# Kernel tuning notes

Hardware: AMD Instinct MI355X
Metric: run time of the kernel (lower is better)

The kernel has to match this reference:

```python
import jax, jax.numpy as jnp
import numpy as np

B, T, N, F_, KH, D, KD = 16, 12, 325, 64, 4, 16, 3  # batch, time, nodes, feat, heads, head_dim, diffusion steps
H = KH // 2
EPS = 1e-5


def setup_inputs() -> dict:
    key = jax.random.key(0)
    ks = jax.random.split(key, 16)
    lin = lambda k: (jax.random.normal(k, (F_, F_), jnp.float32) * 0.02)
    return {
        "x": jax.random.normal(ks[0], (B, T, N, F_), jnp.float32),
        "A": jax.random.uniform(ks[1], (KD, N, N), jnp.float32),
        "AT": jax.random.uniform(ks[2], (KD, N, N), jnp.float32),
        "Wq": lin(ks[3]), "bq": jnp.zeros((F_,), jnp.float32),
        "Wk": lin(ks[4]), "bk": jnp.zeros((F_,), jnp.float32),
        "Wks": lin(ks[5]), "bks": jnp.zeros((F_,), jnp.float32),
        "Wv": lin(ks[6]), "bv": jnp.zeros((F_,), jnp.float32),
        "Wvs": lin(ks[7]), "bvs": jnp.zeros((F_,), jnp.float32),
        "Wdi": jax.random.normal(ks[8], (H, KD, N, N), jnp.float32) * 0.05,
        "Wdo": jax.random.normal(ks[9], (H, KD, N, N), jnp.float32) * 0.05,
        "Wf1": lin(ks[10]), "bf1": jnp.zeros((F_,), jnp.float32),
        "Wf2": lin(ks[11]), "bf2": jnp.zeros((F_,), jnp.float32),
        "g_ln": jnp.ones((F_,), jnp.float32), "b_ln": jnp.zeros((F_,), jnp.float32),
    }


def _heads(y):
    # [B,T,N,F] -> [KH,B,T,N,D]  (torch.split along -1 then stack on dim 0)
    return y.reshape(B, T, N, KH, D).transpose(3, 0, 1, 2, 4)


def _attn_half(q, k, ks_, v, vs, bias):
    # q,k,ks_,v,vs: [H,B,T,N,D]; bias: [H,1,1,N,N]
    scale = 1.0 / jnp.sqrt(jnp.float32(D))
    e = jnp.einsum('hbtnd,hbtmd->hbtnm', q, k) * scale + bias
    es = jax.nn.sigmoid((q * ks_).sum(-1, keepdims=True) * scale)  # [H,B,T,N,1]
    e = e - e.max(-1, keepdims=True)
    ex = jnp.exp(e)
    a = ex / (es + ex.sum(-1, keepdims=True))  # sigmoid-augmented softmax
    out = jnp.einsum('hbtnm,hbtmd->hbtnd', a, v)
    return out + vs - a.sum(-1, keepdims=True) * vs


def reference(x, A, AT, Wq, bq, Wk, bk, Wks, bks, Wv, bv, Wvs, bvs,
              Wdi, Wdo, Wf1, bf1, Wf2, bf2, g_ln, b_ln):
    q = _heads(x @ Wq.T + bq)
    k = _heads(x @ Wk.T + bk)
    ks_ = _heads(x @ Wks.T + bks)
    v = _heads(x @ Wv.T + bv)
    vs = _heads(x @ Wvs.T + bvs)

    # DCN graph-diffusion bias: sum_j W[h,j] * A[j] -> [H,1,1,N,N]
    bias_i = jnp.einsum('hknm,knm->hnm', Wdi, A)[:, None, None]
    bias_o = jnp.einsum('hknm,knm->hnm', Wdo, AT)[:, None, None]

    vi = _attn_half(q[:H], k[:H], ks_[:H], v[:H], vs[:H], bias_i)
    vo = _attn_half(q[H:], k[H:], ks_[H:], v[H:], vs[H:], bias_o)

    val = jnp.concatenate([vi, vo], 0)  # [KH,B,T,N,D]
    val = val.transpose(1, 2, 3, 0, 4).reshape(B, T, N, F_)

    h = jax.nn.gelu(val @ Wf1.T + bf1, approximate=False) @ Wf2.T + bf2
    h = h + x

    mu = h.mean(-1, keepdims=True)
    var = ((h - mu) ** 2).mean(-1, keepdims=True)
    return g_ln * (h - mu) / jnp.sqrt(var + EPS) + b_ln
```

## Files before the change

### kernel.cpp

```cpp
#include <hip/hip_runtime.h>
#include <hip/hip_bf16.h>
#include <math.h>

#define NN 325
#define FD 64
#define KH 4
#define DH 16
#define BT 192
#define NN2 (NN*NN)
#define PST (NN*DH)
#define VTS  352
#define VSLICE (16*VTS)
#define HSTR 72
#define PLW 352
#define NPROJ 975
#define NBIAS 1848
#define NPAD  (KH*BT)
#define LOG2E 1.44269504088896f

typedef __attribute__((ext_vector_type(8))) short short8;
typedef __attribute__((ext_vector_type(4))) float f32x4;

union U8 { uint4 u; short8 s; ushort us[8]; };
__device__ inline short8 lds8(const ushort* p){ U8 t; t.u = *(const uint4*)p; return t.s; }
__device__ inline float b2f(ushort v){ return __uint_as_float(((unsigned)v) << 16); }
__device__ inline ushort f2b(float f){
  unsigned u = __float_as_uint(f);
  u += 0x7fff + ((u >> 16) & 1);
  return (ushort)(u >> 16);
}
__device__ inline unsigned pk2(float a, float b){
  union { __hip_bfloat162 h; unsigned u; } t;
  t.h = __float22bfloat162_rn(float2{a, b});
  return t.u;
}
__device__ inline short8 cvt8(const float* p){
  float4 u = ((const float4*)p)[0], v = ((const float4*)p)[1];
  U8 t;
  t.us[0]=f2b(u.x); t.us[1]=f2b(u.y); t.us[2]=f2b(u.z); t.us[3]=f2b(u.w);
  t.us[4]=f2b(v.x); t.us[5]=f2b(v.y); t.us[6]=f2b(v.z); t.us[7]=f2b(v.w);
  return t.s;
}

__global__ __launch_bounds__(256) void wpack_kernel(
    const float* __restrict__ Wq,  const float* __restrict__ bq,
    const float* __restrict__ Wk,  const float* __restrict__ bk,
    const float* __restrict__ Wks, const float* __restrict__ bks,
    const float* __restrict__ Wv,  const float* __restrict__ bv,
    const float* __restrict__ Wvs, const float* __restrict__ bvs,
    const float* __restrict__ Wf1, const float* __restrict__ Wf2,
    ushort* __restrict__ Wcat, float* __restrict__ bcat,
    ushort* __restrict__ idT){
  int blk = blockIdx.x;
  if (blk == 7){
    for (int e = threadIdx.x; e < 672; e += 256){
      int l = e & 31, mm = l & 15, gg = l >> 4;
      U8 t;
      #pragma unroll
      for (int j = 0; j < 8; ++j) t.us[j] = (mm == gg*8 + j) ? (ushort)0x3F80 : (ushort)0;
      *(uint4*)(idT + (size_t)e*8) = t.u;
    }
    return;
  }
  const float* Ws[7] = {Wq, Wk, Wks, Wv, Wvs, Wf1, Wf2};
  const float* bs[5] = {bq, bk, bks, bv, bvs};
  int f = blk * 64 + (threadIdx.x >> 2);
  int c0 = (threadIdx.x & 3) * 8;
  const float* wr = Ws[blk] + (f & 63) * 64;
  unsigned* dst = (unsigned*)Wcat + f * 32 + c0;
  #pragma unroll
  for (int c = 0; c < 8; ++c)
    dst[c] = f2b(wr[2*(c0+c)]) | ((unsigned)f2b(wr[2*(c0+c)+1]) << 16);
  if (blk < 5 && (threadIdx.x & 3) == 0) bcat[f] = bs[blk][f & 63];
}

__global__ __launch_bounds__(256) void prep_kernel(
    const float* __restrict__ x, const ushort* __restrict__ Wcat,
    const float* __restrict__ bcat, ushort* __restrict__ proj,
    ushort* __restrict__ vt,
    const float* __restrict__ Wdi, const float* __restrict__ Wdo,
    const float* __restrict__ A,   const float* __restrict__ AT,
    ushort* __restrict__ biasB){
  int bid = blockIdx.x, tid = threadIdx.x;
  if (bid < NPROJ){
    int lane = tid & 63, wid = tid >> 6;
    int r0 = bid * 64 + wid * 16;
    int m = lane & 15, g = lane >> 4;
    int gr = r0 + m;
    int bt = gr / NN, n = gr - bt * NN;
    const float* xr = x + (size_t)gr * 64 + g * 8;
    short8 xb0 = cvt8(xr);
    short8 xb1 = cvt8(xr + 32);
    for (int ct = 0; ct < 20; ++ct){
      short8 w0 = lds8(Wcat + ((size_t)(ct*16 + m) * 64 + g * 8));
      short8 w1 = lds8(Wcat + ((size_t)(ct*16 + m) * 64 + g * 8 + 32));
      float4 b4 = *(const float4*)(bcat + ct*16 + 4*g);
      f32x4 acc = {b4.x, b4.y, b4.z, b4.w};
      acc = __builtin_amdgcn_mfma_f32_16x16x32_bf16(w0, xb0, acc, 0, 0, 0);
      acc = __builtin_amdgcn_mfma_f32_16x16x32_bf16(w1, xb1, acc, 0, 0, 0);
      if (ct >= 12 && ct < 16){
        ushort* vs = vt + (size_t)((ct-12)*BT + bt) * VSLICE + n;
        #pragma unroll
        for (int rg = 0; rg < 4; ++rg)
          vs[(size_t)(4*g + rg) * VTS] = f2b(acc[rg]);
      } else {
        float sc = (ct < 4) ? 0.25f * LOG2E : 1.0f;
        uint2 w;
        w.x = pk2(acc[0]*sc, acc[1]*sc);
        w.y = pk2(acc[2]*sc, acc[3]*sc);
        *(uint2*)(proj + ((size_t)ct * BT + bt) * PST + n*16 + 4*g) = w;
      }
    }
  } else if (bid < NPROJ + NBIAS){
    int idx = (bid - NPROJ) * 256 + tid;
    int h = idx / 118272;
    int rem = idx - h * 118272;
    int n = rem / 352, mc = rem - n * 352;
    float s = -1e30f;
    if (n < NN && mc < NN){
      int r = n * NN + mc;
      s = 0.f;
      if (h < 2){
        #pragma unroll
        for (int k = 0; k < 3; ++k) s += Wdi[(h*3 + k)*NN2 + r] * A[k*NN2 + r];
      } else {
        int h2 = h - 2;
        #pragma unroll
        for (int k = 0; k < 3; ++k) s += Wdo[(h2*3 + k)*NN2 + r] * AT[k*NN2 + r];
      }
      s *= LOG2E;
    }
    biasB[idx] = f2b(s);
  } else {
    int slice = bid - NPROJ - NBIAS;
    ushort* vs = vt + (size_t)slice * VSLICE;
    if (tid < 432){
      int d = tid / 27, c = NN + tid % 27;
      vs[(size_t)d * VTS + c] = 0;
    }
  }
}

__global__ __launch_bounds__(256, 3) void attn_kernel(
    const ushort* __restrict__ proj, const ushort* __restrict__ biasB,
    const ushort* __restrict__ idT, const ushort* __restrict__ vt,
    ushort* __restrict__ val){
  __shared__ __align__(16) ushort Pl[4][16*PLW];
  int tid = threadIdx.x, lane = tid & 63, wid = tid >> 6;
  int tile = blockIdx.x * 4 + wid;
  int qt = tile % 21, bh = tile / 21;
  int h = bh / BT, bt = bh - h * BT;
  int m = lane & 15, g = lane >> 4;

  const ushort* qb  = proj + (size_t)((0*KH + h)*BT + bt) * PST;
  const ushort* kb  = proj + (size_t)((1*KH + h)*BT + bt) * PST;
  const ushort* ksb = proj + (size_t)((2*KH + h)*BT + bt) * PST;
  const ushort* vsb = proj + (size_t)((4*KH + h)*BT + bt) * PST;

  const ushort* pa0 = (g < 2) ? (kb + m*16 + g*8) : (idT + (size_t)(lane & 31)*8);
  const ushort* pb0 = (g < 2)
      ? (qb + (size_t)(qt*16 + m)*16 + g*8)
      : (biasB + (size_t)(h*336 + qt*16 + m)*352 + (g-2)*8);
  int bstep = (g < 2) ? 0 : 16;

  ushort* Pw = &Pl[wid][m*PLW + g*4];
  float rowsum = 0.f;
  #pragma unroll
  for (int ct = 0; ct < 21; ++ct){
    short8 a = lds8(pa0 + ct*256);
    short8 b = lds8(pb0 + ct*bstep);
    f32x4 acc = {0.f, 0.f, 0.f, 0.f};
    acc = __builtin_amdgcn_mfma_f32_16x16x32_bf16(a, b, acc, 0, 0, 0);
    float e0 = __builtin_amdgcn_exp2f(acc[0]);
    float e1 = __builtin_amdgcn_exp2f(acc[1]);
    float e2 = __builtin_amdgcn_exp2f(acc[2]);
    float e3 = __builtin_amdgcn_exp2f(acc[3]);
    rowsum += (e0 + e1) + (e2 + e3);
    uint2 w; w.x = pk2(e0, e1); w.y = pk2(e2, e3);
    *(uint2*)(Pw + ct*16) = w;
  }
  { uint2 z; z.x = 0u; z.y = 0u; *(uint2*)(Pw + 336) = z; }

  rowsum += __shfl_xor(rowsum, 16, 64);
  rowsum += __shfl_xor(rowsum, 32, 64);

  int nq = qt*16 + m, nb = min(nq, NN-1);
  uint2 qw = *(const uint2*)(qb + (size_t)nb*16 + g*4);
  uint2 kw = *(const uint2*)(ksb + (size_t)nb*16 + g*4);
  float dp = b2f((ushort)(qw.x & 0xffff)) * b2f((ushort)(kw.x & 0xffff))
           + b2f((ushort)(qw.x >> 16))    * b2f((ushort)(kw.x >> 16))
           + b2f((ushort)(qw.y & 0xffff)) * b2f((ushort)(kw.y & 0xffff))
           + b2f((ushort)(qw.y >> 16))    * b2f((ushort)(kw.y >> 16));
  dp += __shfl_xor(dp, 16, 64);
  dp += __shfl_xor(dp, 32, 64);
  float esv  = __builtin_amdgcn_rcpf(1.f + __builtin_amdgcn_exp2f(-dp));
  float inv  = __builtin_amdgcn_rcpf(esv + rowsum);
  float beta = 1.f - rowsum * inv;

  asm volatile("s_waitcnt lgkmcnt(0)" ::: "memory");

  const ushort* Pr  = &Pl[wid][m*PLW + g*8];
  const ushort* vtg = vt + (size_t)(h*BT + bt)*VSLICE + (size_t)m*VTS + g*8;
  f32x4 o = {0.f, 0.f, 0.f, 0.f};
  #pragma unroll
  for (int tt = 0; tt < 11; ++tt){
    short8 pf = lds8(Pr + tt*32);
    short8 vf = lds8(vtg + tt*32);
    o = __builtin_amdgcn_mfma_f32_16x16x32_bf16(pf, vf, o, 0, 0, 0);
  }

  int sb = g << 4;
  float invr[4], betr[4];
  #pragma unroll
  for (int rg = 0; rg < 4; ++rg){
    invr[rg] = __uint_as_float(__builtin_amdgcn_ds_bpermute(sb + rg*4, __float_as_uint(inv)));
    betr[rg] = __uint_as_float(__builtin_amdgcn_ds_bpermute(sb + rg*4, __float_as_uint(beta)));
  }
  #pragma unroll
  for (int rg = 0; rg < 4; ++rg){
    int n = qt*16 + 4*g + rg;
    int nc = min(n, NN-1);
    float vsx = b2f(vsb[(size_t)nc*16 + m]);
    float res = o[rg]*invr[rg] + betr[rg]*vsx;
    if (n < NN) val[((size_t)bt*NN + n)*FD + h*16 + m] = f2b(res);
  }
}

__global__ __launch_bounds__(256) void ffn_kernel(
    const ushort* __restrict__ val, const float* __restrict__ x,
    const ushort* __restrict__ Wf1b, const float* __restrict__ bf1,
    const ushort* __restrict__ Wf2b, const float* __restrict__ bf2,
    const float* __restrict__ g_ln, const float* __restrict__ b_ln,
    float* __restrict__ out){
  __shared__ ushort hs[4][16 * HSTR];
  int tid = threadIdx.x, lane = tid & 63, wid = tid >> 6;
  int m = lane & 15, g = lane >> 4;
  int r0 = blockIdx.x * 64 + wid * 16;
  int row = r0 + m;

  short8 vb0 = lds8(val + ((size_t)row * 64 + g * 8));
  short8 vb1 = lds8(val + ((size_t)row * 64 + g * 8 + 32));

  #pragma unroll
  for (int ct = 0; ct < 4; ++ct){
    short8 w0 = lds8(Wf1b + ((size_t)(ct*16 + m) * 64 + g * 8));
    short8 w1 = lds8(Wf1b + ((size_t)(ct*16 + m) * 64 + g * 8 + 32));
    float4 b4 = *(const float4*)(bf1 + ct*16 + 4*g);
    f32x4 acc = {b4.x, b4.y, b4.z, b4.w};
    acc = __builtin_amdgcn_mfma_f32_16x16x32_bf16(w0, vb0, acc, 0, 0, 0);
    acc = __builtin_amdgcn_mfma_f32_16x16x32_bf16(w1, vb1, acc, 0, 0, 0);
    uint2 w;
    float g0 = 0.5f*acc[0]*(1.f + erff(acc[0]*0.70710678118654752f));
    float g1 = 0.5f*acc[1]*(1.f + erff(acc[1]*0.70710678118654752f));
    float g2 = 0.5f*acc[2]*(1.f + erff(acc[2]*0.70710678118654752f));
    float g3 = 0.5f*acc[3]*(1.f + erff(acc[3]*0.70710678118654752f));
    w.x = pk2(g0, g1); w.y = pk2(g2, g3);
    *(uint2*)&hs[wid][m * HSTR + ct*16 + 4*g] = w;
  }
  asm volatile("s_waitcnt lgkmcnt(0)" ::: "memory");
  short8 h0 = lds8(&hs[wid][m * HSTR + g * 8]);
  short8 h1 = lds8(&hs[wid][m * HSTR + g * 8 + 32]);

  float t[4][4];
  #pragma unroll
  for (int ct = 0; ct < 4; ++ct){
    short8 w0 = lds8(Wf2b + ((size_t)(ct*16 + m) * 64 + g * 8));
    short8 w1 = lds8(Wf2b + ((size_t)(ct*16 + m) * 64 + g * 8 + 32));
    float4 b4 = *(const float4*)(bf2 + ct*16 + 4*g);
    f32x4 acc = {b4.x, b4.y, b4.z, b4.w};
    acc = __builtin_amdgcn_mfma_f32_16x16x32_bf16(w0, h0, acc, 0, 0, 0);
    acc = __builtin_amdgcn_mfma_f32_16x16x32_bf16(w1, h1, acc, 0, 0, 0);
    float4 xr = *(const float4*)(x + (size_t)row * 64 + ct*16 + 4*g);
    t[ct][0] = acc[0] + xr.x; t[ct][1] = acc[1] + xr.y;
    t[ct][2] = acc[2] + xr.z; t[ct][3] = acc[3] + xr.w;
  }
  float s = 0.f;
  #pragma unroll
  for (int ct = 0; ct < 4; ++ct) s += (t[ct][0]+t[ct][1]) + (t[ct][2]+t[ct][3]);
  s += __shfl_xor(s, 16, 64); s += __shfl_xor(s, 32, 64);
  float mu = s * (1.f/64.f);
  float v = 0.f;
  #pragma unroll
  for (int ct = 0; ct < 4; ++ct){
    #pragma unroll
    for (int rg = 0; rg < 4; ++rg){ float d = t[ct][rg] - mu; v += d*d; }
  }
  v += __shfl_xor(v, 16, 64); v += __shfl_xor(v, 32, 64);
  float rs = rsqrtf(v * (1.f/64.f) + 1e-5f);
  #pragma unroll
  for (int ct = 0; ct < 4; ++ct){
    float4 g4 = *(const float4*)(g_ln + ct*16 + 4*g);
    float4 bb = *(const float4*)(b_ln + ct*16 + 4*g);
    float4 o;
    o.x = g4.x*(t[ct][0]-mu)*rs + bb.x;
    o.y = g4.y*(t[ct][1]-mu)*rs + bb.y;
    o.z = g4.z*(t[ct][2]-mu)*rs + bb.z;
    o.w = g4.w*(t[ct][3]-mu)*rs + bb.w;
    *(float4*)(out + (size_t)row * 64 + ct*16 + 4*g) = o;
  }
}

extern "C" void kernel_launch(void* const* d_in, const int* in_sizes, int n_in,
                              void* d_out, int out_size, void* d_ws, size_t ws_size,
                              hipStream_t stream) {
  const float* x    = (const float*)d_in[0];
  const float* A    = (const float*)d_in[1];
  const float* AT   = (const float*)d_in[2];
  const float* Wq   = (const float*)d_in[3];
  const float* bq   = (const float*)d_in[4];
  const float* Wk   = (const float*)d_in[5];
  const float* bk   = (const float*)d_in[6];
  const float* Wks  = (const float*)d_in[7];
  const float* bks  = (const float*)d_in[8];
  const float* Wv   = (const float*)d_in[9];
  const float* bv   = (const float*)d_in[10];
  const float* Wvs  = (const float*)d_in[11];
  const float* bvs  = (const float*)d_in[12];
  const float* Wdi  = (const float*)d_in[13];
  const float* Wdo  = (const float*)d_in[14];
  const float* Wf1  = (const float*)d_in[15];
  const float* bf1  = (const float*)d_in[16];
  const float* Wf2  = (const float*)d_in[17];
  const float* bf2  = (const float*)d_in[18];
  const float* g_ln = (const float*)d_in[19];
  const float* b_ln = (const float*)d_in[20];
  float* out = (float*)d_out;

  float* ws = (float*)d_ws;
  ushort* proj  = (ushort*)ws;
  ushort* biasB = (ushort*)(ws + 9984000);
  ushort* idT   = biasB + 473088;
  ushort* val   = (ushort*)(ws + 10441600);
  ushort* vt    = (ushort*)(ws + 12438400);
  ushort* Wcat  = (ushort*)(ws + 14601088);
  float*  bcat  = ws + 14615424;
  ushort* Wf1b  = Wcat + 320*64;
  ushort* Wf2b  = Wcat + 384*64;

  wpack_kernel<<<8, 256, 0, stream>>>(Wq, bq, Wk, bk, Wks, bks,
                                      Wv, bv, Wvs, bvs, Wf1, Wf2, Wcat, bcat, idT);
  prep_kernel<<<NPROJ + NBIAS + NPAD, 256, 0, stream>>>(
      x, Wcat, bcat, proj, vt, Wdi, Wdo, A, AT, biasB);
  attn_kernel<<<4032, 256, 0, stream>>>(proj, biasB, idT, vt, val);
  ffn_kernel<<<975, 256, 0, stream>>>(val, x, Wf1b, bf1, Wf2b, bf2,
                                      g_ln, b_ln, out);
}
```

Baseline: 193.3 us.

## Prefetch attention operands, swizzle LDS P tile, shrink blocks and swizzle block order

The attention kernel now runs 2 waves per block instead of 4 and remaps block indices with an XCD-style swizzle. V fragments and the q/ks loads are issued early into registers. The QK MFMA loop is software-pipelined two iterations ahead. The P tile in LDS uses an XOR column swizzle to cut bank conflicts between the write and read patterns. The aim is to hide global-load latency and LDS conflicts, at the cost of higher register pressure under the new launch bounds.

```diff
diff --git a/kernel.cpp b/kernel.cpp
--- a/kernel.cpp
+++ b/kernel.cpp
@@ -16,6 +16,7 @@
 #define NPROJ 975
 #define NBIAS 1848
 #define NPAD  (KH*BT)
+#define ANB   8064
 #define LOG2E 1.44269504088896f
 
 typedef __attribute__((ext_vector_type(8))) short short8;
@@ -141,21 +142,33 @@
   }
 }
 
-__global__ __launch_bounds__(256, 3) void attn_kernel(
+__global__ __launch_bounds__(128, 4) void attn_kernel(
     const ushort* __restrict__ proj, const ushort* __restrict__ biasB,
     const ushort* __restrict__ idT, const ushort* __restrict__ vt,
     ushort* __restrict__ val){
-  __shared__ __align__(16) ushort Pl[4][16*PLW];
+  __shared__ __align__(16) ushort Pl[2][16*PLW];
   int tid = threadIdx.x, lane = tid & 63, wid = tid >> 6;
-  int tile = blockIdx.x * 4 + wid;
+  int bid = (int)blockIdx.x;
+  int swz = (bid & 7) * (ANB/8) + (bid >> 3);
+  int tile = swz * 2 + wid;
   int qt = tile % 21, bh = tile / 21;
   int h = bh / BT, bt = bh - h * BT;
   int m = lane & 15, g = lane >> 4;
+  int sxf = (m & 7) << 3, sxt = (m & 3) << 3;
 
   const ushort* qb  = proj + (size_t)((0*KH + h)*BT + bt) * PST;
   const ushort* kb  = proj + (size_t)((1*KH + h)*BT + bt) * PST;
   const ushort* ksb = proj + (size_t)((2*KH + h)*BT + bt) * PST;
   const ushort* vsb = proj + (size_t)((4*KH + h)*BT + bt) * PST;
+
+  const ushort* vtg = vt + (size_t)(h*BT + bt)*VSLICE + (size_t)m*VTS + g*8;
+  short8 vf[11];
+  #pragma unroll
+  for (int tt = 0; tt < 8; ++tt) vf[tt] = lds8(vtg + tt*32);
+
+  int nq = qt*16 + m, nb = min(nq, NN-1);
+  uint2 qw = *(const uint2*)(qb + (size_t)nb*16 + g*4);
+  uint2 kw = *(const uint2*)(ksb + (size_t)nb*16 + g*4);
 
   const ushort* pa0 = (g < 2) ? (kb + m*16 + g*8) : (idT + (size_t)(lane & 31)*8);
   const ushort* pb0 = (g < 2)
@@ -163,30 +176,35 @@
       : (biasB + (size_t)(h*336 + qt*16 + m)*352 + (g-2)*8);
   int bstep = (g < 2) ? 0 : 16;
 
-  ushort* Pw = &Pl[wid][m*PLW + g*4];
+  ushort* Pw = &Pl[wid][m*PLW];
   float rowsum = 0.f;
+  short8 zero = {0,0,0,0,0,0,0,0};
+  short8 a0 = lds8(pa0),       b0 = lds8(pb0);
+  short8 a1 = lds8(pa0 + 256), b1 = lds8(pb0 + bstep);
   #pragma unroll
   for (int ct = 0; ct < 21; ++ct){
-    short8 a = lds8(pa0 + ct*256);
-    short8 b = lds8(pb0 + ct*bstep);
+    short8 a2 = zero, b2 = zero;
+    if (ct + 2 < 21){ a2 = lds8(pa0 + (ct+2)*256); b2 = lds8(pb0 + (ct+2)*bstep); }
     f32x4 acc = {0.f, 0.f, 0.f, 0.f};
-    acc = __builtin_amdgcn_mfma_f32_16x16x32_bf16(a, b, acc, 0, 0, 0);
+    acc = __builtin_amdgcn_mfma_f32_16x16x32_bf16(a0, b0, acc, 0, 0, 0);
     float e0 = __builtin_amdgcn_exp2f(acc[0]);
     float e1 = __builtin_amdgcn_exp2f(acc[1]);
     float e2 = __builtin_amdgcn_exp2f(acc[2]);
     float e3 = __builtin_amdgcn_exp2f(acc[3]);
     rowsum += (e0 + e1) + (e2 + e3);
     uint2 w; w.x = pk2(e0, e1); w.y = pk2(e2, e3);
-    *(uint2*)(Pw + ct*16) = w;
-  }
-  { uint2 z; z.x = 0u; z.y = 0u; *(uint2*)(Pw + 336) = z; }
+    int col = ct*16 + g*4;
+    *(uint2*)(Pw + (col ^ (ct < 20 ? sxf : sxt))) = w;
+    a0 = a1; b0 = b1; a1 = a2; b1 = b2;
+  }
+  { uint2 z; z.x = 0u; z.y = 0u; *(uint2*)(Pw + ((336 + g*4) ^ sxt)) = z; }
+
+  #pragma unroll
+  for (int tt = 8; tt < 11; ++tt) vf[tt] = lds8(vtg + tt*32);
 
   rowsum += __shfl_xor(rowsum, 16, 64);
   rowsum += __shfl_xor(rowsum, 32, 64);
 
-  int nq = qt*16 + m, nb = min(nq, NN-1);
-  uint2 qw = *(const uint2*)(qb + (size_t)nb*16 + g*4);
-  uint2 kw = *(const uint2*)(ksb + (size_t)nb*16 + g*4);
   float dp = b2f((ushort)(qw.x & 0xffff)) * b2f((ushort)(kw.x & 0xffff))
            + b2f((ushort)(qw.x >> 16))    * b2f((ushort)(kw.x >> 16))
            + b2f((ushort)(qw.y & 0xffff)) * b2f((ushort)(kw.y & 0xffff))
@@ -199,14 +217,13 @@
 
   asm volatile("s_waitcnt lgkmcnt(0)" ::: "memory");
 
-  const ushort* Pr  = &Pl[wid][m*PLW + g*8];
-  const ushort* vtg = vt + (size_t)(h*BT + bt)*VSLICE + (size_t)m*VTS + g*8;
+  const ushort* Pr = &Pl[wid][m*PLW];
   f32x4 o = {0.f, 0.f, 0.f, 0.f};
   #pragma unroll
   for (int tt = 0; tt < 11; ++tt){
-    short8 pf = lds8(Pr + tt*32);
-    short8 vf = lds8(vtg + tt*32);
-    o = __builtin_amdgcn_mfma_f32_16x16x32_bf16(pf, vf, o, 0, 0, 0);
+    int col = tt*32 + g*8;
+    short8 pf = lds8(Pr + (col ^ (tt < 10 ? sxf : sxt)));
+    o = __builtin_amdgcn_mfma_f32_16x16x32_bf16(pf, vf[tt], o, 0, 0, 0);
   }
 
   int sb = g << 4;
@@ -341,7 +358,7 @@
                                       Wv, bv, Wvs, bvs, Wf1, Wf2, Wcat, bcat, idT);
   prep_kernel<<<NPROJ + NBIAS + NPAD, 256, 0, stream>>>(
       x, Wcat, bcat, proj, vt, Wdi, Wdo, A, AT, biasB);
-  attn_kernel<<<4032, 256, 0, stream>>>(proj, biasB, idT, vt, val);
+  attn_kernel<<<ANB, 128, 0, stream>>>(proj, biasB, idT, vt, val);
   ffn_kernel<<<975, 256, 0, stream>>>(val, x, Wf1b, bf1, Wf2b, bf2,
                                       g_ln, b_ln, out);
 }
```

Result: no change. 195.4 us (+1.1%).

## Keep attention probabilities in registers by permuting key order to match MFMA layout

Applied to the files above, without the earlier changes.

The attention kernel no longer stages exponentiated scores through shared memory. Key tokens are permuted, in both the bias layout and the K-row addressing, so that two QK MFMA outputs pack directly into the A-operand layout of the PV MFMA. The kernel also prefetches the V fragments and the next QK operands into registers, swizzles block order, and raises the occupancy hint to 4. This removes LDS writes and reads plus the wait between them, at the cost of higher register pressure and more complex index mapping.

```diff
diff --git a/kernel.cpp b/kernel.cpp
--- a/kernel.cpp
+++ b/kernel.cpp
@@ -12,10 +12,10 @@
 #define VTS  352
 #define VSLICE (16*VTS)
 #define HSTR 72
-#define PLW 352
 #define NPROJ 975
 #define NBIAS 1848
 #define NPAD  (KH*BT)
+#define ANB   4032
 #define LOG2E 1.44269504088896f
 
 typedef __attribute__((ext_vector_type(8))) short short8;
@@ -116,17 +116,19 @@
     int h = idx / 118272;
     int rem = idx - h * 118272;
     int n = rem / 352, mc = rem - n * 352;
+    int j = mc >> 4, r = mc & 15;
+    int tok = 32*(j>>1) + 8*(r>>2) + 4*(j&1) + (r&3);
     float s = -1e30f;
-    if (n < NN && mc < NN){
-      int r = n * NN + mc;
+    if (n < NN && tok < NN){
+      int ridx = n * NN + tok;
       s = 0.f;
       if (h < 2){
         #pragma unroll
-        for (int k = 0; k < 3; ++k) s += Wdi[(h*3 + k)*NN2 + r] * A[k*NN2 + r];
+        for (int k = 0; k < 3; ++k) s += Wdi[(h*3 + k)*NN2 + ridx] * A[k*NN2 + ridx];
       } else {
         int h2 = h - 2;
         #pragma unroll
-        for (int k = 0; k < 3; ++k) s += Wdo[(h2*3 + k)*NN2 + r] * AT[k*NN2 + r];
+        for (int k = 0; k < 3; ++k) s += Wdo[(h2*3 + k)*NN2 + ridx] * AT[k*NN2 + ridx];
       }
       s *= LOG2E;
     }
@@ -141,52 +143,81 @@
   }
 }
 
-__global__ __launch_bounds__(256, 3) void attn_kernel(
+__global__ __launch_bounds__(256, 4) void attn_kernel(
     const ushort* __restrict__ proj, const ushort* __restrict__ biasB,
     const ushort* __restrict__ idT, const ushort* __restrict__ vt,
     ushort* __restrict__ val){
-  __shared__ __align__(16) ushort Pl[4][16*PLW];
   int tid = threadIdx.x, lane = tid & 63, wid = tid >> 6;
-  int tile = blockIdx.x * 4 + wid;
+  int bid = (int)blockIdx.x;
+  int swz = (bid & 7) * (ANB/8) + (bid >> 3);
+  int tile = swz * 4 + wid;
   int qt = tile % 21, bh = tile / 21;
   int h = bh / BT, bt = bh - h * BT;
   int m = lane & 15, g = lane >> 4;
+  int lext = 8*(m >> 2) + (m & 3);
 
   const ushort* qb  = proj + (size_t)((0*KH + h)*BT + bt) * PST;
   const ushort* kb  = proj + (size_t)((1*KH + h)*BT + bt) * PST;
   const ushort* ksb = proj + (size_t)((2*KH + h)*BT + bt) * PST;
   const ushort* vsb = proj + (size_t)((4*KH + h)*BT + bt) * PST;
 
-  const ushort* pa0 = (g < 2) ? (kb + m*16 + g*8) : (idT + (size_t)(lane & 31)*8);
-  const ushort* pb0 = (g < 2)
+  const ushort* vtg = vt + (size_t)(h*BT + bt)*VSLICE + (size_t)m*VTS + g*8;
+  short8 vf[11];
+  #pragma unroll
+  for (int tt = 0; tt < 11; ++tt) vf[tt] = lds8(vtg + tt*32);
+
+  int nq = qt*16 + m, nb = min(nq, NN-1);
+  uint2 qw = *(const uint2*)(qb + (size_t)nb*16 + g*4);
+  uint2 kw = *(const uint2*)(ksb + (size_t)nb*16 + g*4);
+
+  const ushort* abase = (g < 2) ? (kb + g*8) : (idT + (size_t)(lane & 31)*8);
+  int amul = (g < 2) ? 16 : 0;
+  const ushort* pbase = (g < 2)
       ? (qb + (size_t)(qt*16 + m)*16 + g*8)
       : (biasB + (size_t)(h*336 + qt*16 + m)*352 + (g-2)*8);
   int bstep = (g < 2) ? 0 : 16;
 
-  ushort* Pw = &Pl[wid][m*PLW + g*4];
+  short8 aE0 = lds8(abase + min(lext, 324)*amul);
+  short8 aO0 = lds8(abase + min(lext + 4, 324)*amul);
+  short8 bE0 = lds8(pbase);
+  short8 bO0 = lds8(pbase + bstep);
+
+  f32x4 o = {0.f, 0.f, 0.f, 0.f};
   float rowsum = 0.f;
   #pragma unroll
-  for (int ct = 0; ct < 21; ++ct){
-    short8 a = lds8(pa0 + ct*256);
-    short8 b = lds8(pb0 + ct*bstep);
-    f32x4 acc = {0.f, 0.f, 0.f, 0.f};
-    acc = __builtin_amdgcn_mfma_f32_16x16x32_bf16(a, b, acc, 0, 0, 0);
-    float e0 = __builtin_amdgcn_exp2f(acc[0]);
-    float e1 = __builtin_amdgcn_exp2f(acc[1]);
-    float e2 = __builtin_amdgcn_exp2f(acc[2]);
-    float e3 = __builtin_amdgcn_exp2f(acc[3]);
-    rowsum += (e0 + e1) + (e2 + e3);
-    uint2 w; w.x = pk2(e0, e1); w.y = pk2(e2, e3);
-    *(uint2*)(Pw + ct*16) = w;
-  }
-  { uint2 z; z.x = 0u; z.y = 0u; *(uint2*)(Pw + 336) = z; }
+  for (int tt = 0; tt < 11; ++tt){
+    short8 aE1 = aE0, aO1 = aO0, bE1 = bE0, bO1 = bO0;
+    if (tt < 10){
+      int wbase = 32*(tt+1);
+      aE1 = lds8(abase + min(wbase + lext,     324)*amul);
+      aO1 = lds8(abase + min(wbase + lext + 4, 324)*amul);
+      bE1 = lds8(pbase + (2*tt+2)*bstep);
+      bO1 = lds8(pbase + (2*tt+3)*bstep);
+    }
+    f32x4 accE = {0.f,0.f,0.f,0.f}, accO = {0.f,0.f,0.f,0.f};
+    accE = __builtin_amdgcn_mfma_f32_16x16x32_bf16(aE0, bE0, accE, 0, 0, 0);
+    accO = __builtin_amdgcn_mfma_f32_16x16x32_bf16(aO0, bO0, accO, 0, 0, 0);
+    float e0 = __builtin_amdgcn_exp2f(accE[0]);
+    float e1 = __builtin_amdgcn_exp2f(accE[1]);
+    float e2 = __builtin_amdgcn_exp2f(accE[2]);
+    float e3 = __builtin_amdgcn_exp2f(accE[3]);
+    float e4 = __builtin_amdgcn_exp2f(accO[0]);
+    float e5 = __builtin_amdgcn_exp2f(accO[1]);
+    float e6 = __builtin_amdgcn_exp2f(accO[2]);
+    float e7 = __builtin_amdgcn_exp2f(accO[3]);
+    rowsum += ((e0 + e1) + (e2 + e3)) + ((e4 + e5) + (e6 + e7));
+    U8 pf;
+    pf.u.x = pk2(e0, e1);
+    pf.u.y = pk2(e2, e3);
+    pf.u.z = pk2(e4, e5);
+    pf.u.w = pk2(e6, e7);
+    o = __builtin_amdgcn_mfma_f32_16x16x32_bf16(pf.s, vf[tt], o, 0, 0, 0);
+    aE0 = aE1; aO0 = aO1; bE0 = bE1; bO0 = bO1;
+  }
 
   rowsum += __shfl_xor(rowsum, 16, 64);
   rowsum += __shfl_xor(rowsum, 32, 64);
 
-  int nq = qt*16 + m, nb = min(nq, NN-1);
-  uint2 qw = *(const uint2*)(qb + (size_t)nb*16 + g*4);
-  uint2 kw = *(const uint2*)(ksb + (size_t)nb*16 + g*4);
   float dp = b2f((ushort)(qw.x & 0xffff)) * b2f((ushort)(kw.x & 0xffff))
            + b2f((ushort)(qw.x >> 16))    * b2f((ushort)(kw.x >> 16))
            + b2f((ushort)(qw.y & 0xffff)) * b2f((ushort)(kw.y & 0xffff))
@@ -196,18 +227,6 @@
   float esv  = __builtin_amdgcn_rcpf(1.f + __builtin_amdgcn_exp2f(-dp));
   float inv  = __builtin_amdgcn_rcpf(esv + rowsum);
   float beta = 1.f - rowsum * inv;
-
-  asm volatile("s_waitcnt lgkmcnt(0)" ::: "memory");
-
-  const ushort* Pr  = &Pl[wid][m*PLW + g*8];
-  const ushort* vtg = vt + (size_t)(h*BT + bt)*VSLICE + (size_t)m*VTS + g*8;
-  f32x4 o = {0.f, 0.f, 0.f, 0.f};
-  #pragma unroll
-  for (int tt = 0; tt < 11; ++tt){
-    short8 pf = lds8(Pr + tt*32);
-    short8 vf = lds8(vtg + tt*32);
-    o = __builtin_amdgcn_mfma_f32_16x16x32_bf16(pf, vf, o, 0, 0, 0);
-  }
 
   int sb = g << 4;
   float invr[4], betr[4];
@@ -341,7 +360,7 @@
                                       Wv, bv, Wvs, bvs, Wf1, Wf2, Wcat, bcat, idT);
   prep_kernel<<<NPROJ + NBIAS + NPAD, 256, 0, stream>>>(
       x, Wcat, bcat, proj, vt, Wdi, Wdo, A, AT, biasB);
-  attn_kernel<<<4032, 256, 0, stream>>>(proj, biasB, idT, vt, val);
+  attn_kernel<<<ANB, 256, 0, stream>>>(proj, biasB, idT, vt, val);
   ffn_kernel<<<975, 256, 0, stream>>>(val, x, Wf1b, bf1, Wf2b, bf2,
                                       g_ln, b_ln, out);
 }
```

Result: no change. 194.8 us (+0.8%).
